# Kernel tuning notes

Hardware: AMD Instinct MI355X
Metric: run time of the kernel (lower is better)

The kernel has to match this reference:

```python
import jax, jax.numpy as jnp
import numpy as np

B, S, E, HEAD = 8, 2048, 512, 64  # head_size = embeddings_dims // no_of_heads = 512 // 8


def setup_inputs() -> dict:
    key = jax.random.key(0)
    kx, kq, kk, kv, kl = jax.random.split(key, 5)
    x = jax.random.normal(kx, (B, S, E), dtype=jnp.float32)
    # Linear(512 -> 64, bias=False); store as [E, HEAD] so y = x @ W
    Wq = jax.random.normal(kq, (E, HEAD), dtype=jnp.float32) * (E ** -0.5)
    Wk = jax.random.normal(kk, (E, HEAD), dtype=jnp.float32) * (E ** -0.5)
    Wv = jax.random.normal(kv, (E, HEAD), dtype=jnp.float32) * (E ** -0.5)
    # Realistic padding mask: 1 for first `length` tokens, 0 after.
    lengths = jax.random.randint(kl, (B,), S // 2, S + 1)
    mask = (jnp.arange(S)[None, :] < lengths[:, None]).astype(jnp.int32)
    return {"x": x, "Wq": Wq, "Wk": Wk, "Wv": Wv, "mask": mask}


def reference(x, Wq, Wk, Wv, mask):
    # q, k, v: [B, S, HEAD]
    q = x @ Wq
    k = x @ Wk
    v = x @ Wv
    # scores: [B, S, S], scaled by head_size**-0.5 (k.shape[-1] in the original)
    scores = jnp.einsum('bqd,bkd->bqk', q, k) * (HEAD ** -0.5)
    causal = jnp.tril(jnp.ones((S, S), dtype=bool))            # [S, S]
    keep = (mask[:, None, :] != 0) & causal[None, :, :]        # padding mask broadcast over query rows, then causal
    scores = jnp.where(keep, scores, -jnp.inf)
    attn = jax.nn.softmax(scores, axis=-1)                     # [B, S, S]
    out = attn @ v                                             # [B, S, HEAD]
    return out
```

## Files before the change

kernel.cpp:

```cpp
#include <hip/hip_runtime.h>

#define BB 8
#define SS 2048
#define EE 512
#define HD 64
#define CHUNK 256
#define KT 64
#define NCH 8
#define TST 72
#define PS32 36
#define XRS 40
#define XKB 1280
#define NITEMS 576

typedef __attribute__((ext_vector_type(8))) short bf16x8;
typedef __attribute__((ext_vector_type(4))) float f32x4;

static __device__ __forceinline__ unsigned short f2bf(float f) {
    unsigned u = __builtin_bit_cast(unsigned, f);
    u = (u + 0x7fffu + ((u >> 16) & 1u)) >> 16;
    return (unsigned short)u;
}
static __device__ __forceinline__ float bf2f(unsigned short h) {
    unsigned u = ((unsigned)h) << 16;
    return __builtin_bit_cast(float, u);
}
static __device__ __forceinline__ unsigned pack2(float lo, float hi) {
    unsigned ulo = __builtin_bit_cast(unsigned, lo) >> 16;
    unsigned uhi = __builtin_bit_cast(unsigned, hi) & 0xffff0000u;
    return uhi | ulo;
}

__global__ __launch_bounds__(256) void pack_w_kernel(
    const float* __restrict__ Wq, const float* __restrict__ Wk, const float* __restrict__ Wv,
    unsigned short* __restrict__ Wt) {
    int tid = blockIdx.x * 256 + threadIdx.x;
    if (tid >= 3 * EE * HD) return;
    int w_idx = tid / (EE * HD);
    int rem = tid % (EE * HD);
    int kk = rem / HD, n = rem % HD;
    const float* Wsrc = (w_idx == 0) ? Wq : ((w_idx == 1) ? Wk : Wv);
    float val = Wsrc[kk * HD + n];
    if (w_idx == 0) val *= 0.125f;
    int kb = kk >> 5, kr = kk & 31, quad = kr >> 3, j = kr & 7;
    int t = n >> 4, c = n & 15;
    int lane = quad * 16 + c;
    Wt[w_idx * (EE * HD) + ((kb * 4 + t) * 64 + lane) * 8 + j] = f2bf(val);
}

__global__ __launch_bounds__(256) void qkv_kernel(
    const float* __restrict__ x,
    const unsigned short* __restrict__ Wt,
    unsigned short* __restrict__ q,
    unsigned short* __restrict__ k,
    unsigned short* __restrict__ vT) {
    __shared__ __align__(16) unsigned short Xs[16 * XKB];
    const int tid = threadIdx.x;
    const int lane = tid & 63;
    const int t = tid >> 6;
    const int c = lane & 15, quad = lane >> 4;
    const int r0 = blockIdx.x * 32;

    const float* xt = x + (size_t)r0 * EE;
#pragma unroll
    for (int i = 0; i < 16; ++i) {
        int fi = i * 256 + tid;
        int e4 = fi * 4;
        float4 v4 = *(const float4*)(xt + e4);
        int row = e4 >> 9, col = e4 & 511;
        int kb = col >> 5, cc = col & 31;
        ushort4 pk;
        pk.x = f2bf(v4.x); pk.y = f2bf(v4.y); pk.z = f2bf(v4.z); pk.w = f2bf(v4.w);
        *(ushort4*)(&Xs[kb * XKB + row * XRS + cc]) = pk;
    }
    __syncthreads();

    f32x4 acc[2][3];
#pragma unroll
    for (int rt = 0; rt < 2; ++rt)
        for (int m = 0; m < 3; ++m) acc[rt][m] = (f32x4){0.f, 0.f, 0.f, 0.f};

    const unsigned short* wbase0 = Wt + t * 512 + lane * 8;
#pragma unroll
    for (int kb = 0; kb < EE / 32; ++kb) {
        const unsigned short* wb = wbase0 + kb * 2048;
        bf16x8 wfrag[3];
#pragma unroll
        for (int m = 0; m < 3; ++m) wfrag[m] = *(const bf16x8*)(wb + m * (EE * HD));
#pragma unroll
        for (int rt = 0; rt < 2; ++rt) {
            bf16x8 xfrag = *(const bf16x8*)(&Xs[kb * XKB + (rt * 16 + c) * XRS + quad * 8]);
#pragma unroll
            for (int m = 0; m < 3; ++m)
                acc[rt][m] = __builtin_amdgcn_mfma_f32_16x16x32_bf16(wfrag[m], xfrag, acc[rt][m], 0, 0, 0);
        }
    }

    const int colq = t * 16 + quad * 4;
#pragma unroll
    for (int rt = 0; rt < 2; ++rt) {
        const int row = r0 + rt * 16 + c;
        ushort4 pq, pkk;
        pq.x = f2bf(acc[rt][0][0]); pq.y = f2bf(acc[rt][0][1]);
        pq.z = f2bf(acc[rt][0][2]); pq.w = f2bf(acc[rt][0][3]);
        pkk.x = f2bf(acc[rt][1][0]); pkk.y = f2bf(acc[rt][1][1]);
        pkk.z = f2bf(acc[rt][1][2]); pkk.w = f2bf(acc[rt][1][3]);
        *(ushort4*)(q + (size_t)row * HD + colq) = pq;
        *(ushort4*)(k + (size_t)row * HD + colq) = pkk;
        int b_ = row >> 11, sb = row & (SS - 1);
#pragma unroll
        for (int r = 0; r < 4; ++r)
            vT[((size_t)b_ * HD + colq + r) * SS + sb] = f2bf(acc[rt][2][r]);
    }
}

__global__ __launch_bounds__(256, 3) void attn_kernel(
    const unsigned short* __restrict__ q,
    const unsigned short* __restrict__ k,
    const unsigned short* __restrict__ vT,
    const int* __restrict__ mask,
    unsigned short* __restrict__ po,
    float* __restrict__ pl,
    float* __restrict__ out) {
    __shared__ __align__(16) unsigned short Ks[2][64 * TST];
    __shared__ __align__(16) unsigned short Vs[2][64 * TST];
    __shared__ __align__(16) unsigned int Ps32[4][16 * PS32];
    const int tid = threadIdx.x;
    const int lane = tid & 63, wave = tid >> 6;
    const int c = lane & 15, quad = lane >> 4;

    int t = NITEMS - 1 - blockIdx.x;
    const int b_ = t / 72;
    int r = t % 72;
    int g = 0;
    while ((g + 1) * (g + 2) <= r) ++g;
    int rr = r - g * (g + 1);
    const int Q = 2 * g + rr / (g + 1);
    const int cx = rr % (g + 1);
    const int kstart = cx * CHUNK;
    const int kend = min(kstart + CHUNK, Q * 128 + 128);
    const int ntiles = (kend - kstart) >> 6;
    const int nch_active = Q / 2 + 1;
    const int r0 = Q * 128 + wave * 32;

    const unsigned short* qb_p = q + (size_t)b_ * SS * HD;
    const unsigned short* kb_p = k + (size_t)b_ * SS * HD;
    const unsigned short* vb = vT + (size_t)b_ * HD * SS;
    const int* mb = mask + b_ * SS;

    bf16x8 aq[2][2];
#pragma unroll
    for (int rt = 0; rt < 2; ++rt) {
        const unsigned short* qrow = qb_p + (size_t)(r0 + rt * 16 + c) * HD + quad * 8;
        aq[rt][0] = *(const bf16x8*)(qrow);
        aq[rt][1] = *(const bf16x8*)(qrow + 32);
    }

    f32x4 o[2][4];
    float l_part[2] = {0.f, 0.f};
#pragma unroll
    for (int rt = 0; rt < 2; ++rt)
        for (int tt = 0; tt < 4; ++tt) o[rt][tt] = (f32x4){0.f, 0.f, 0.f, 0.f};

    bf16x8 sk[2], sv[2];
    auto stage_load = [&](int k0) {
        const unsigned short* ksrc = kb_p + (size_t)k0 * HD;
#pragma unroll
        for (int rnd = 0; rnd < 2; ++rnd) {
            int e = (rnd * 256 + tid) * 8;
            sk[rnd] = *(const bf16x8*)(ksrc + e);
            int t8 = rnd * 256 + tid;
            int vr = t8 >> 3, vc = (t8 & 7) * 8;
            sv[rnd] = *(const bf16x8*)(vb + (size_t)vr * SS + k0 + vc);
        }
    };
    auto stage_write = [&](int buf) {
        unsigned short* kd = &Ks[buf][0];
        unsigned short* vd = &Vs[buf][0];
#pragma unroll
        for (int rnd = 0; rnd < 2; ++rnd) {
            int e = (rnd * 256 + tid) * 8;
            int krow = e >> 6, kcol = e & 63;
            *(bf16x8*)(kd + krow * TST + kcol) = sk[rnd];
            int t8 = rnd * 256 + tid;
            int vr = t8 >> 3, vc = (t8 & 7) * 8;
            *(bf16x8*)(vd + vr * TST + vc) = sv[rnd];
        }
    };

    stage_load(kstart);
    stage_write(0);
    for (int kt = 0; kt < ntiles; ++kt) {
        __syncthreads();
        const int k0 = kstart + kt * KT;
        const bool pre = (kt + 1 < ntiles);
        if (pre) stage_load(k0 + KT);
        const unsigned short* ks = &Ks[kt & 1][0];
        const unsigned short* vs = &Vs[kt & 1][0];

        int mks[4][4];
#pragma unroll
        for (int kg = 0; kg < 4; ++kg) {
            int4 mv = *(const int4*)(mb + k0 + kg * 16 + quad * 4);
            mks[kg][0] = mv.x; mks[kg][1] = mv.y; mks[kg][2] = mv.z; mks[kg][3] = mv.w;
        }

        bf16x8 kf[4][2];
#pragma unroll
        for (int kg = 0; kg < 4; ++kg) {
            kf[kg][0] = *(const bf16x8*)(ks + (kg * 16 + c) * TST + quad * 8);
            kf[kg][1] = *(const bf16x8*)(ks + (kg * 16 + c) * TST + 32 + quad * 8);
        }

        bf16x8 pB[2][2];
#pragma unroll
        for (int rt = 0; rt < 2; ++rt) {
            const int rbase = r0 + rt * 16;
            const int qr = rbase + c;
            const bool fullc = (k0 + KT <= rbase);
            f32x4 accs4[4];
            __builtin_amdgcn_s_setprio(1);
#pragma unroll
            for (int kg = 0; kg < 4; ++kg) {
                f32x4 a = (f32x4){0.f, 0.f, 0.f, 0.f};
                a = __builtin_amdgcn_mfma_f32_16x16x32_bf16(kf[kg][0], aq[rt][0], a, 0, 0, 0);
                a = __builtin_amdgcn_mfma_f32_16x16x32_bf16(kf[kg][1], aq[rt][1], a, 0, 0, 0);
                accs4[kg] = a;
            }
            __builtin_amdgcn_s_setprio(0);
            unsigned int* pb = &Ps32[wave][0];
#pragma unroll
            for (int kg = 0; kg < 4; ++kg) {
                float pe[4];
#pragma unroll
                for (int rr2 = 0; rr2 < 4; ++rr2) {
                    int key = k0 + kg * 16 + quad * 4 + rr2;
                    bool keep = (mks[kg][rr2] != 0) && (fullc || key <= qr);
                    float e = __expf(fminf(accs4[kg][rr2], 80.f));
                    float p = keep ? e : 0.f;
                    l_part[rt] += p;
                    pe[rr2] = p;
                }
                uint2 w2;
                w2.x = pack2(pe[0], pe[1]);
                w2.y = pack2(pe[2], pe[3]);
                *(uint2*)(pb + c * PS32 + kg * 8 + quad * 2) = w2;
            }
            const unsigned short* pb16 = (const unsigned short*)pb;
            pB[rt][0] = *(const bf16x8*)(pb16 + c * (PS32 * 2) + quad * 8);
            pB[rt][1] = *(const bf16x8*)(pb16 + c * (PS32 * 2) + 32 + quad * 8);
        }

#pragma unroll
        for (int tt = 0; tt < 4; ++tt) {
            bf16x8 bv0 = *(const bf16x8*)(vs + (tt * 16 + c) * TST + quad * 8);
            bf16x8 bv1 = *(const bf16x8*)(vs + (tt * 16 + c) * TST + 32 + quad * 8);
            __builtin_amdgcn_s_setprio(1);
#pragma unroll
            for (int rt = 0; rt < 2; ++rt) {
                o[rt][tt] = __builtin_amdgcn_mfma_f32_16x16x32_bf16(bv0, pB[rt][0], o[rt][tt], 0, 0, 0);
                o[rt][tt] = __builtin_amdgcn_mfma_f32_16x16x32_bf16(bv1, pB[rt][1], o[rt][tt], 0, 0, 0);
            }
            __builtin_amdgcn_s_setprio(0);
        }

        if (pre) stage_write((kt + 1) & 1);
    }

    float lv[2];
#pragma unroll
    for (int rt = 0; rt < 2; ++rt) {
        float s = l_part[rt];
        s += __shfl_xor(s, 16);
        s += __shfl_xor(s, 32);
        lv[rt] = s;
    }

    if (nch_active == 1) {
#pragma unroll
        for (int rt = 0; rt < 2; ++rt) {
            int row = r0 + rt * 16 + c;
            float l = lv[rt];
            float inv = (l > 0.f) ? 1.f / l : 0.f;
#pragma unroll
            for (int tt = 0; tt < 4; ++tt) {
                float4 o4;
                o4.x = o[rt][tt][0] * inv; o4.y = o[rt][tt][1] * inv;
                o4.z = o[rt][tt][2] * inv; o4.w = o[rt][tt][3] * inv;
                *(float4*)(out + ((size_t)b_ * SS + row) * HD + tt * 16 + quad * 4) = o4;
            }
        }
        return;
    }

#pragma unroll
    for (int rt = 0; rt < 2; ++rt) {
        int row_abs = r0 + rt * 16 + c;
        int qb_i = row_abs >> 6, rl = row_abs & 63;
        size_t base = (size_t)(b_ * 32 + qb_i) * NCH + cx;
        float l = lv[rt];
        float inv = (l > 0.f) ? 1.f / l : 0.f;
#pragma unroll
        for (int tt = 0; tt < 4; ++tt) {
            ushort4 pk;
            pk.x = f2bf(o[rt][tt][0] * inv); pk.y = f2bf(o[rt][tt][1] * inv);
            pk.z = f2bf(o[rt][tt][2] * inv); pk.w = f2bf(o[rt][tt][3] * inv);
            *(ushort4*)(po + base * 4096 + (size_t)rl * 64 + tt * 16 + quad * 4) = pk;
        }
        if (quad == 0) pl[base * 64 + rl] = l;
    }
}

__global__ __launch_bounds__(256) void combine_kernel(
    const unsigned short* __restrict__ po,
    const float* __restrict__ pl,
    float* __restrict__ out) {
    int t = blockIdx.x * 256 + threadIdx.x;
    if (t >= BB * (SS - 256) * (HD / 4)) return;
    int d4 = (t & 15) * 4;
    int rg = t >> 4;
    int b_ = rg / (SS - 256);
    int row = 256 + rg % (SS - 256);
    int qb = row >> 6, rl = row & 63;
    int nch = row / CHUNK + 1;
    size_t base = (size_t)(b_ * 32 + qb) * NCH;
    float L = 0.f;
    float acc0 = 0.f, acc1 = 0.f, acc2 = 0.f, acc3 = 0.f;
    for (int cc = 0; cc < nch; ++cc) {
        float l = pl[(base + cc) * 64 + rl];
        L += l;
        ushort4 pk = *(const ushort4*)(po + (base + cc) * 4096 + (size_t)rl * 64 + d4);
        acc0 += l * bf2f(pk.x);
        acc1 += l * bf2f(pk.y);
        acc2 += l * bf2f(pk.z);
        acc3 += l * bf2f(pk.w);
    }
    float inv = (L > 0.f) ? 1.f / L : 0.f;
    float4 o4;
    o4.x = acc0 * inv; o4.y = acc1 * inv; o4.z = acc2 * inv; o4.w = acc3 * inv;
    *(float4*)(out + ((size_t)b_ * SS + row) * HD + d4) = o4;
}

extern "C" void kernel_launch(void* const* d_in, const int* in_sizes, int n_in,
                              void* d_out, int out_size, void* d_ws, size_t ws_size,
                              hipStream_t stream) {
    const float* x = (const float*)d_in[0];
    const float* Wq = (const float*)d_in[1];
    const float* Wk = (const float*)d_in[2];
    const float* Wv = (const float*)d_in[3];
    const int* mask = (const int*)d_in[4];
    float* out = (float*)d_out;

    unsigned short* ws = (unsigned short*)d_ws;
    unsigned short* Wt = ws;
    unsigned short* q = Wt + 3 * EE * HD;
    unsigned short* kk = q + (size_t)BB * SS * HD;
    unsigned short* vT = kk + (size_t)BB * SS * HD;
    unsigned short* po = vT + (size_t)BB * SS * HD;
    float* pl = (float*)(po + (size_t)BB * 32 * NCH * 4096);

    pack_w_kernel<<<dim3((3 * EE * HD + 255) / 256), dim3(256), 0, stream>>>(Wq, Wk, Wv, Wt);
    qkv_kernel<<<dim3(BB * SS / 32), dim3(256), 0, stream>>>(x, Wt, q, kk, vT);
    attn_kernel<<<dim3(NITEMS), dim3(256), 0, stream>>>(q, kk, vT, mask, po, pl, out);
    combine_kernel<<<dim3((BB * (SS - 256) * (HD / 4) + 255) / 256), dim3(256), 0, stream>>>(po, pl, out);
}
```

Baseline: 109.9 us.

## Skip padded key tiles, load K fragments directly, and coalesce V-transpose stores

```diff
diff --git a/kernel.cpp b/kernel.cpp
--- a/kernel.cpp
+++ b/kernel.cpp
@@ -11,6 +11,7 @@
 #define PS32 36
 #define XRS 40
 #define XKB 1280
+#define VTR 66
 #define NITEMS 576
 
 typedef __attribute__((ext_vector_type(8))) short bf16x8;
@@ -107,10 +108,26 @@
         pkk.z = f2bf(acc[rt][1][2]); pkk.w = f2bf(acc[rt][1][3]);
         *(ushort4*)(q + (size_t)row * HD + colq) = pq;
         *(ushort4*)(k + (size_t)row * HD + colq) = pkk;
-        int b_ = row >> 11, sb = row & (SS - 1);
-#pragma unroll
-        for (int r = 0; r < 4; ++r)
-            vT[((size_t)b_ * HD + colq + r) * SS + sb] = f2bf(acc[rt][2][r]);
+    }
+
+    __syncthreads();
+    unsigned short* Vt = Xs;
+#pragma unroll
+    for (int rt = 0; rt < 2; ++rt) {
+        int rowl = rt * 16 + c;
+        ushort4 pv;
+        pv.x = f2bf(acc[rt][2][0]); pv.y = f2bf(acc[rt][2][1]);
+        pv.z = f2bf(acc[rt][2][2]); pv.w = f2bf(acc[rt][2][3]);
+        *(ushort4*)(&Vt[rowl * VTR + colq]) = pv;
+    }
+    __syncthreads();
+    {
+        int d = tid >> 2, ch = tid & 3;
+        unsigned short tmp[8];
+#pragma unroll
+        for (int j = 0; j < 8; ++j) tmp[j] = Vt[(ch * 8 + j) * VTR + d];
+        int b_ = r0 >> 11, sb = (r0 & (SS - 1)) + ch * 8;
+        *(bf16x8*)(vT + ((size_t)b_ * HD + d) * SS + sb) = *(const bf16x8*)tmp;
     }
 }
 
@@ -122,7 +139,6 @@
     unsigned short* __restrict__ po,
     float* __restrict__ pl,
     float* __restrict__ out) {
-    __shared__ __align__(16) unsigned short Ks[2][64 * TST];
     __shared__ __align__(16) unsigned short Vs[2][64 * TST];
     __shared__ __align__(16) unsigned int Ps32[4][16 * PS32];
     const int tid = threadIdx.x;
@@ -148,6 +164,11 @@
     const unsigned short* vb = vT + (size_t)b_ * HD * SS;
     const int* mb = mask + b_ * SS;
 
+    int ntl = 0;
+#pragma unroll
+    for (int i = 0; i < 4; ++i)
+        if (i < ntiles && mb[kstart + i * KT] != 0) ntl = i + 1;
+
     bf16x8 aq[2][2];
 #pragma unroll
     for (int rt = 0; rt < 2; ++rt) {
@@ -162,109 +183,121 @@
     for (int rt = 0; rt < 2; ++rt)
         for (int tt = 0; tt < 4; ++tt) o[rt][tt] = (f32x4){0.f, 0.f, 0.f, 0.f};
 
-    bf16x8 sk[2], sv[2];
+    bf16x8 sv[2];
     auto stage_load = [&](int k0) {
-        const unsigned short* ksrc = kb_p + (size_t)k0 * HD;
 #pragma unroll
         for (int rnd = 0; rnd < 2; ++rnd) {
-            int e = (rnd * 256 + tid) * 8;
-            sk[rnd] = *(const bf16x8*)(ksrc + e);
             int t8 = rnd * 256 + tid;
             int vr = t8 >> 3, vc = (t8 & 7) * 8;
             sv[rnd] = *(const bf16x8*)(vb + (size_t)vr * SS + k0 + vc);
         }
     };
     auto stage_write = [&](int buf) {
-        unsigned short* kd = &Ks[buf][0];
         unsigned short* vd = &Vs[buf][0];
 #pragma unroll
         for (int rnd = 0; rnd < 2; ++rnd) {
-            int e = (rnd * 256 + tid) * 8;
-            int krow = e >> 6, kcol = e & 63;
-            *(bf16x8*)(kd + krow * TST + kcol) = sk[rnd];
             int t8 = rnd * 256 + tid;
             int vr = t8 >> 3, vc = (t8 & 7) * 8;
             *(bf16x8*)(vd + vr * TST + vc) = sv[rnd];
         }
     };
 
-    stage_load(kstart);
-    stage_write(0);
-    for (int kt = 0; kt < ntiles; ++kt) {
-        __syncthreads();
-        const int k0 = kstart + kt * KT;
-        const bool pre = (kt + 1 < ntiles);
-        if (pre) stage_load(k0 + KT);
-        const unsigned short* ks = &Ks[kt & 1][0];
-        const unsigned short* vs = &Vs[kt & 1][0];
-
-        int mks[4][4];
-#pragma unroll
-        for (int kg = 0; kg < 4; ++kg) {
-            int4 mv = *(const int4*)(mb + k0 + kg * 16 + quad * 4);
-            mks[kg][0] = mv.x; mks[kg][1] = mv.y; mks[kg][2] = mv.z; mks[kg][3] = mv.w;
-        }
-
-        bf16x8 kf[4][2];
-#pragma unroll
-        for (int kg = 0; kg < 4; ++kg) {
-            kf[kg][0] = *(const bf16x8*)(ks + (kg * 16 + c) * TST + quad * 8);
-            kf[kg][1] = *(const bf16x8*)(ks + (kg * 16 + c) * TST + 32 + quad * 8);
-        }
-
-        bf16x8 pB[2][2];
-#pragma unroll
-        for (int rt = 0; rt < 2; ++rt) {
-            const int rbase = r0 + rt * 16;
-            const int qr = rbase + c;
-            const bool fullc = (k0 + KT <= rbase);
-            f32x4 accs4[4];
-            __builtin_amdgcn_s_setprio(1);
+    if (ntl > 0) {
+        stage_load(kstart);
+        stage_write(0);
+        for (int kt = 0; kt < ntl; ++kt) {
+            __syncthreads();
+            const int k0 = kstart + kt * KT;
+            const bool pre = (kt + 1 < ntl);
+            if (pre) stage_load(k0 + KT);
+            const unsigned short* vs = &Vs[kt & 1][0];
+            const bool vall = (mb[k0 + KT - 1] != 0);
+
+            bf16x8 kf[4][2];
 #pragma unroll
             for (int kg = 0; kg < 4; ++kg) {
-                f32x4 a = (f32x4){0.f, 0.f, 0.f, 0.f};
-                a = __builtin_amdgcn_mfma_f32_16x16x32_bf16(kf[kg][0], aq[rt][0], a, 0, 0, 0);
-                a = __builtin_amdgcn_mfma_f32_16x16x32_bf16(kf[kg][1], aq[rt][1], a, 0, 0, 0);
-                accs4[kg] = a;
+                const unsigned short* krow = kb_p + (size_t)(k0 + kg * 16 + c) * HD + quad * 8;
+                kf[kg][0] = *(const bf16x8*)(krow);
+                kf[kg][1] = *(const bf16x8*)(krow + 32);
             }
-            __builtin_amdgcn_s_setprio(0);
-            unsigned int* pb = &Ps32[wave][0];
-#pragma unroll
-            for (int kg = 0; kg < 4; ++kg) {
-                float pe[4];
-#pragma unroll
-                for (int rr2 = 0; rr2 < 4; ++rr2) {
-                    int key = k0 + kg * 16 + quad * 4 + rr2;
-                    bool keep = (mks[kg][rr2] != 0) && (fullc || key <= qr);
-                    float e = __expf(fminf(accs4[kg][rr2], 80.f));
-                    float p = keep ? e : 0.f;
-                    l_part[rt] += p;
-                    pe[rr2] = p;
+
+            bf16x8 pB[2][2];
+#pragma unroll
+            for (int rt = 0; rt < 2; ++rt) {
+                const int rbase = r0 + rt * 16;
+                const int qr = rbase + c;
+                const bool fullc = (k0 + KT <= rbase);
+                f32x4 accs4[4];
+                __builtin_amdgcn_s_setprio(1);
+#pragma unroll
+                for (int kg = 0; kg < 4; ++kg) {
+                    f32x4 a = (f32x4){0.f, 0.f, 0.f, 0.f};
+                    a = __builtin_amdgcn_mfma_f32_16x16x32_bf16(kf[kg][0], aq[rt][0], a, 0, 0, 0);
+                    a = __builtin_amdgcn_mfma_f32_16x16x32_bf16(kf[kg][1], aq[rt][1], a, 0, 0, 0);
+                    accs4[kg] = a;
                 }
-                uint2 w2;
-                w2.x = pack2(pe[0], pe[1]);
-                w2.y = pack2(pe[2], pe[3]);
-                *(uint2*)(pb + c * PS32 + kg * 8 + quad * 2) = w2;
+                __builtin_amdgcn_s_setprio(0);
+                unsigned int* pb = &Ps32[wave][0];
+                if (fullc && vall) {
+#pragma unroll
+                    for (int kg = 0; kg < 4; ++kg) {
+                        float pe[4];
+#pragma unroll
+                        for (int rr2 = 0; rr2 < 4; ++rr2) {
+                            float p = __expf(fminf(accs4[kg][rr2], 80.f));
+                            l_part[rt] += p;
+                            pe[rr2] = p;
+                        }
+                        uint2 w2;
+                        w2.x = pack2(pe[0], pe[1]);
+                        w2.y = pack2(pe[2], pe[3]);
+                        *(uint2*)(pb + c * PS32 + kg * 8 + quad * 2) = w2;
+                    }
+                } else {
+                    int mks[4][4];
+#pragma unroll
+                    for (int kg = 0; kg < 4; ++kg) {
+                        int4 mv = *(const int4*)(mb + k0 + kg * 16 + quad * 4);
+                        mks[kg][0] = mv.x; mks[kg][1] = mv.y; mks[kg][2] = mv.z; mks[kg][3] = mv.w;
+                    }
+#pragma unroll
+                    for (int kg = 0; kg < 4; ++kg) {
+                        float pe[4];
+#pragma unroll
+                        for (int rr2 = 0; rr2 < 4; ++rr2) {
+                            int key = k0 + kg * 16 + quad * 4 + rr2;
+                            bool keep = (mks[kg][rr2] != 0) && (fullc || key <= qr);
+                            float e = __expf(fminf(accs4[kg][rr2], 80.f));
+                            float p = keep ? e : 0.f;
+                            l_part[rt] += p;
+                            pe[rr2] = p;
+                        }
+                        uint2 w2;
+                        w2.x = pack2(pe[0], pe[1]);
+                        w2.y = pack2(pe[2], pe[3]);
+                        *(uint2*)(pb + c * PS32 + kg * 8 + quad * 2) = w2;
+                    }
+                }
+                const unsigned short* pb16 = (const unsigned short*)pb;
+                pB[rt][0] = *(const bf16x8*)(pb16 + c * (PS32 * 2) + quad * 8);
+                pB[rt][1] = *(const bf16x8*)(pb16 + c * (PS32 * 2) + 32 + quad * 8);
             }
-            const unsigned short* pb16 = (const unsigned short*)pb;
-            pB[rt][0] = *(const bf16x8*)(pb16 + c * (PS32 * 2) + quad * 8);
-            pB[rt][1] = *(const bf16x8*)(pb16 + c * (PS32 * 2) + 32 + quad * 8);
-        }
-
-#pragma unroll
-        for (int tt = 0; tt < 4; ++tt) {
-            bf16x8 bv0 = *(const bf16x8*)(vs + (tt * 16 + c) * TST + quad * 8);
-            bf16x8 bv1 = *(const bf16x8*)(vs + (tt * 16 + c) * TST + 32 + quad * 8);
-            __builtin_amdgcn_s_setprio(1);
-#pragma unroll
-            for (int rt = 0; rt < 2; ++rt) {
-                o[rt][tt] = __builtin_amdgcn_mfma_f32_16x16x32_bf16(bv0, pB[rt][0], o[rt][tt], 0, 0, 0);
-                o[rt][tt] = __builtin_amdgcn_mfma_f32_16x16x32_bf16(bv1, pB[rt][1], o[rt][tt], 0, 0, 0);
+
+#pragma unroll
+            for (int tt = 0; tt < 4; ++tt) {
+                bf16x8 bv0 = *(const bf16x8*)(vs + (tt * 16 + c) * TST + quad * 8);
+                bf16x8 bv1 = *(const bf16x8*)(vs + (tt * 16 + c) * TST + 32 + quad * 8);
+                __builtin_amdgcn_s_setprio(1);
+#pragma unroll
+                for (int rt = 0; rt < 2; ++rt) {
+                    o[rt][tt] = __builtin_amdgcn_mfma_f32_16x16x32_bf16(bv0, pB[rt][0], o[rt][tt], 0, 0, 0);
+                    o[rt][tt] = __builtin_amdgcn_mfma_f32_16x16x32_bf16(bv1, pB[rt][1], o[rt][tt], 0, 0, 0);
+                }
+                __builtin_amdgcn_s_setprio(0);
             }
-            __builtin_amdgcn_s_setprio(0);
-        }
-
-        if (pre) stage_write((kt + 1) & 1);
+
+            if (pre) stage_write((kt + 1) & 1);
+        }
     }
 
     float lv[2];
```

Result: slower. 113.8 us (+3.6%).

## Skip fully padded key tiles, fast-path unmasked tiles, vectorize V-transpose store

Applied to the files above, without the earlier changes.

```diff
diff --git a/kernel.cpp b/kernel.cpp
--- a/kernel.cpp
+++ b/kernel.cpp
@@ -90,13 +90,14 @@
 #pragma unroll
         for (int rt = 0; rt < 2; ++rt) {
             bf16x8 xfrag = *(const bf16x8*)(&Xs[kb * XKB + (rt * 16 + c) * XRS + quad * 8]);
-#pragma unroll
-            for (int m = 0; m < 3; ++m)
-                acc[rt][m] = __builtin_amdgcn_mfma_f32_16x16x32_bf16(wfrag[m], xfrag, acc[rt][m], 0, 0, 0);
+            acc[rt][0] = __builtin_amdgcn_mfma_f32_16x16x32_bf16(wfrag[0], xfrag, acc[rt][0], 0, 0, 0);
+            acc[rt][1] = __builtin_amdgcn_mfma_f32_16x16x32_bf16(wfrag[1], xfrag, acc[rt][1], 0, 0, 0);
+            acc[rt][2] = __builtin_amdgcn_mfma_f32_16x16x32_bf16(xfrag, wfrag[2], acc[rt][2], 0, 0, 0);
         }
     }
 
     const int colq = t * 16 + quad * 4;
+    const int colv = t * 16 + c;
 #pragma unroll
     for (int rt = 0; rt < 2; ++rt) {
         const int row = r0 + rt * 16 + c;
@@ -107,10 +108,12 @@
         pkk.z = f2bf(acc[rt][1][2]); pkk.w = f2bf(acc[rt][1][3]);
         *(ushort4*)(q + (size_t)row * HD + colq) = pq;
         *(ushort4*)(k + (size_t)row * HD + colq) = pkk;
-        int b_ = row >> 11, sb = row & (SS - 1);
-#pragma unroll
-        for (int r = 0; r < 4; ++r)
-            vT[((size_t)b_ * HD + colq + r) * SS + sb] = f2bf(acc[rt][2][r]);
+        const int vrow = r0 + rt * 16 + quad * 4;
+        int b_ = vrow >> 11, sb = vrow & (SS - 1);
+        ushort4 pv;
+        pv.x = f2bf(acc[rt][2][0]); pv.y = f2bf(acc[rt][2][1]);
+        pv.z = f2bf(acc[rt][2][2]); pv.w = f2bf(acc[rt][2][3]);
+        *(ushort4*)(vT + ((size_t)b_ * HD + colv) * SS + sb) = pv;
     }
 }
 
@@ -148,6 +151,11 @@
     const unsigned short* vb = vT + (size_t)b_ * HD * SS;
     const int* mb = mask + b_ * SS;
 
+    int ntl = 0;
+#pragma unroll
+    for (int i = 0; i < 4; ++i)
+        if (i < ntiles && mb[kstart + i * KT] != 0) ntl = i + 1;
+
     bf16x8 aq[2][2];
 #pragma unroll
     for (int rt = 0; rt < 2; ++rt) {
@@ -188,83 +196,102 @@
         }
     };
 
-    stage_load(kstart);
-    stage_write(0);
-    for (int kt = 0; kt < ntiles; ++kt) {
-        __syncthreads();
-        const int k0 = kstart + kt * KT;
-        const bool pre = (kt + 1 < ntiles);
-        if (pre) stage_load(k0 + KT);
-        const unsigned short* ks = &Ks[kt & 1][0];
-        const unsigned short* vs = &Vs[kt & 1][0];
-
-        int mks[4][4];
-#pragma unroll
-        for (int kg = 0; kg < 4; ++kg) {
-            int4 mv = *(const int4*)(mb + k0 + kg * 16 + quad * 4);
-            mks[kg][0] = mv.x; mks[kg][1] = mv.y; mks[kg][2] = mv.z; mks[kg][3] = mv.w;
-        }
-
-        bf16x8 kf[4][2];
-#pragma unroll
-        for (int kg = 0; kg < 4; ++kg) {
-            kf[kg][0] = *(const bf16x8*)(ks + (kg * 16 + c) * TST + quad * 8);
-            kf[kg][1] = *(const bf16x8*)(ks + (kg * 16 + c) * TST + 32 + quad * 8);
-        }
-
-        bf16x8 pB[2][2];
-#pragma unroll
-        for (int rt = 0; rt < 2; ++rt) {
-            const int rbase = r0 + rt * 16;
-            const int qr = rbase + c;
-            const bool fullc = (k0 + KT <= rbase);
-            f32x4 accs4[4];
-            __builtin_amdgcn_s_setprio(1);
+    if (ntl > 0) {
+        stage_load(kstart);
+        stage_write(0);
+        for (int kt = 0; kt < ntl; ++kt) {
+            __syncthreads();
+            const int k0 = kstart + kt * KT;
+            const bool pre = (kt + 1 < ntl);
+            if (pre) stage_load(k0 + KT);
+            const unsigned short* ks = &Ks[kt & 1][0];
+            const unsigned short* vs = &Vs[kt & 1][0];
+            const bool vall = (mb[k0 + KT - 1] != 0);
+
+            bf16x8 kf[4][2];
 #pragma unroll
             for (int kg = 0; kg < 4; ++kg) {
-                f32x4 a = (f32x4){0.f, 0.f, 0.f, 0.f};
-                a = __builtin_amdgcn_mfma_f32_16x16x32_bf16(kf[kg][0], aq[rt][0], a, 0, 0, 0);
-                a = __builtin_amdgcn_mfma_f32_16x16x32_bf16(kf[kg][1], aq[rt][1], a, 0, 0, 0);
-                accs4[kg] = a;
+                kf[kg][0] = *(const bf16x8*)(ks + (kg * 16 + c) * TST + quad * 8);
+                kf[kg][1] = *(const bf16x8*)(ks + (kg * 16 + c) * TST + 32 + quad * 8);
             }
-            __builtin_amdgcn_s_setprio(0);
-            unsigned int* pb = &Ps32[wave][0];
-#pragma unroll
-            for (int kg = 0; kg < 4; ++kg) {
-                float pe[4];
-#pragma unroll
-                for (int rr2 = 0; rr2 < 4; ++rr2) {
-                    int key = k0 + kg * 16 + quad * 4 + rr2;
-                    bool keep = (mks[kg][rr2] != 0) && (fullc || key <= qr);
-                    float e = __expf(fminf(accs4[kg][rr2], 80.f));
-                    float p = keep ? e : 0.f;
-                    l_part[rt] += p;
-                    pe[rr2] = p;
+
+            bf16x8 pB[2][2];
+#pragma unroll
+            for (int rt = 0; rt < 2; ++rt) {
+                const int rbase = r0 + rt * 16;
+                const int qr = rbase + c;
+                const bool fullc = (k0 + KT <= rbase);
+                f32x4 accs4[4];
+                __builtin_amdgcn_s_setprio(1);
+#pragma unroll
+                for (int kg = 0; kg < 4; ++kg) {
+                    f32x4 a = (f32x4){0.f, 0.f, 0.f, 0.f};
+                    a = __builtin_amdgcn_mfma_f32_16x16x32_bf16(kf[kg][0], aq[rt][0], a, 0, 0, 0);
+                    a = __builtin_amdgcn_mfma_f32_16x16x32_bf16(kf[kg][1], aq[rt][1], a, 0, 0, 0);
+                    accs4[kg] = a;
                 }
-                uint2 w2;
-                w2.x = pack2(pe[0], pe[1]);
-                w2.y = pack2(pe[2], pe[3]);
-                *(uint2*)(pb + c * PS32 + kg * 8 + quad * 2) = w2;
+                __builtin_amdgcn_s_setprio(0);
+                unsigned int* pb = &Ps32[wave][0];
+                if (fullc && vall) {
+#pragma unroll
+                    for (int kg = 0; kg < 4; ++kg) {
+                        float pe[4];
+#pragma unroll
+                        for (int rr2 = 0; rr2 < 4; ++rr2) {
+                            float p = __expf(fminf(accs4[kg][rr2], 80.f));
+                            l_part[rt] += p;
+                            pe[rr2] = p;
+                        }
+                        uint2 w2;
+                        w2.x = pack2(pe[0], pe[1]);
+                        w2.y = pack2(pe[2], pe[3]);
+                        *(uint2*)(pb + c * PS32 + kg * 8 + quad * 2) = w2;
+                    }
+                } else {
+                    int mks[4][4];
+#pragma unroll
+                    for (int kg = 0; kg < 4; ++kg) {
+                        int4 mv = *(const int4*)(mb + k0 + kg * 16 + quad * 4);
+                        mks[kg][0] = mv.x; mks[kg][1] = mv.y; mks[kg][2] = mv.z; mks[kg][3] = mv.w;
+                    }
+#pragma unroll
+                    for (int kg = 0; kg < 4; ++kg) {
+                        float pe[4];
+#pragma unroll
+                        for (int rr2 = 0; rr2 < 4; ++rr2) {
+                            int key = k0 + kg * 16 + quad * 4 + rr2;
+                            bool keep = (mks[kg][rr2] != 0) && (fullc || key <= qr);
+                            float e = __expf(fminf(accs4[kg][rr2], 80.f));
+                            float p = keep ? e : 0.f;
+                            l_part[rt] += p;
+                            pe[rr2] = p;
+                        }
+                        uint2 w2;
+                        w2.x = pack2(pe[0], pe[1]);
+                        w2.y = pack2(pe[2], pe[3]);
+                        *(uint2*)(pb + c * PS32 + kg * 8 + quad * 2) = w2;
+                    }
+                }
+                const unsigned short* pb16 = (const unsigned short*)pb;
+                pB[rt][0] = *(const bf16x8*)(pb16 + c * (PS32 * 2) + quad * 8);
+                pB[rt][1] = *(const bf16x8*)(pb16 + c * (PS32 * 2) + 32 + quad * 8);
             }
-            const unsigned short* pb16 = (const unsigned short*)pb;
-            pB[rt][0] = *(const bf16x8*)(pb16 + c * (PS32 * 2) + quad * 8);
-            pB[rt][1] = *(const bf16x8*)(pb16 + c * (PS32 * 2) + 32 + quad * 8);
-        }
-
-#pragma unroll
-        for (int tt = 0; tt < 4; ++tt) {
-            bf16x8 bv0 = *(const bf16x8*)(vs + (tt * 16 + c) * TST + quad * 8);
-            bf16x8 bv1 = *(const bf16x8*)(vs + (tt * 16 + c) * TST + 32 + quad * 8);
-            __builtin_amdgcn_s_setprio(1);
-#pragma unroll
-            for (int rt = 0; rt < 2; ++rt) {
-                o[rt][tt] = __builtin_amdgcn_mfma_f32_16x16x32_bf16(bv0, pB[rt][0], o[rt][tt], 0, 0, 0);
-                o[rt][tt] = __builtin_amdgcn_mfma_f32_16x16x32_bf16(bv1, pB[rt][1], o[rt][tt], 0, 0, 0);
+
+#pragma unroll
+            for (int tt = 0; tt < 4; ++tt) {
+                bf16x8 bv0 = *(const bf16x8*)(vs + (tt * 16 + c) * TST + quad * 8);
+                bf16x8 bv1 = *(const bf16x8*)(vs + (tt * 16 + c) * TST + 32 + quad * 8);
+                __builtin_amdgcn_s_setprio(1);
+#pragma unroll
+                for (int rt = 0; rt < 2; ++rt) {
+                    o[rt][tt] = __builtin_amdgcn_mfma_f32_16x16x32_bf16(bv0, pB[rt][0], o[rt][tt], 0, 0, 0);
+                    o[rt][tt] = __builtin_amdgcn_mfma_f32_16x16x32_bf16(bv1, pB[rt][1], o[rt][tt], 0, 0, 0);
+                }
+                __builtin_amdgcn_s_setprio(0);
             }
-            __builtin_amdgcn_s_setprio(0);
-        }
-
-        if (pre) stage_write((kt + 1) & 1);
+
+            if (pre) stage_write((kt + 1) & 1);
+        }
     }
 
     float lv[2];
```

Result: no change. 111.4 us (+1.4%).
